# Kernel optimization log

Measured on AMD Instinct MI355X. Metric: run time of the kernel, lower is better.

## Reference

```python
import jax, jax.numpy as jnp
import numpy as np

NUM_LAYERS = 2
VOCAB = 32000
INPUT = 1024
HIDDEN = 1024
OUTPUT = 32000
BATCH = 8
SEQ = 256


def setup_inputs() -> dict:
    key = jax.random.key(0)
    ks = jax.random.split(key, 8)
    s_in = 1.0 / np.sqrt(INPUT)
    s_h = 1.0 / np.sqrt(HIDDEN)
    input_ = jax.random.randint(ks[0], (BATCH, SEQ), 0, VOCAB)
    emb = jax.random.normal(ks[1], (VOCAB, INPUT), jnp.float32)
    # Gate order along last dim: [i, f, g, o], each of width HIDDEN.
    Wx = jax.random.uniform(ks[2], (NUM_LAYERS, INPUT, 4 * HIDDEN), jnp.float32, -s_in, s_in)
    bx = jax.random.uniform(ks[3], (NUM_LAYERS, 4 * HIDDEN), jnp.float32, -s_in, s_in)
    Wh = jax.random.uniform(ks[4], (NUM_LAYERS, HIDDEN, 4 * HIDDEN), jnp.float32, -s_h, s_h)
    bh = jax.random.uniform(ks[5], (NUM_LAYERS, 4 * HIDDEN), jnp.float32, -s_h, s_h)
    Wd = jax.random.uniform(ks[6], (HIDDEN, OUTPUT), jnp.float32, -s_h, s_h)
    bd = jax.random.uniform(ks[7], (OUTPUT,), jnp.float32, -s_h, s_h)
    return {"input_": input_, "emb": emb, "Wx": Wx, "bx": bx, "Wh": Wh, "bh": bh, "Wd": Wd, "bd": bd}


def _lstm_core(input_, emb, Wx, bx, Wh, bh, Wd, bd):
    x = emb[input_]                      # [B, T, E]
    xs = jnp.swapaxes(x, 0, 1)           # [T, B, E]
    h0 = jnp.zeros((NUM_LAYERS, x.shape[0], HIDDEN), x.dtype)
    c0 = jnp.zeros_like(h0)

    def step(carry, x_t):
        h, c = carry
        layer_in = x_t
        new_h, new_c = [], []
        for l in range(NUM_LAYERS):
            gates = layer_in @ Wx[l] + bx[l] + h[l] @ Wh[l] + bh[l]  # [B, 4H]
            i_g, f_g, g_g, o_g = jnp.split(gates, 4, axis=-1)
            i_g = jax.nn.sigmoid(i_g)
            f_g = jax.nn.sigmoid(f_g)
            o_g = jax.nn.sigmoid(o_g)
            g_g = jnp.tanh(g_g)
            c_l = f_g * c[l] + i_g * g_g
            h_l = o_g * jnp.tanh(c_l)
            new_h.append(h_l)
            new_c.append(c_l)
            layer_in = h_l
        return (jnp.stack(new_h), jnp.stack(new_c)), layer_in

    (_, _), tops = jax.lax.scan(step, (h0, c0), xs)  # tops: [T, B, H]
    out = tops @ Wd + bd                              # [T, B, V]
    return jnp.swapaxes(out, 0, 1)                    # [B, T, V]


def reference(input_, emb, Wx, bx, Wh, bh, Wd, bd):
    return _lstm_core(input_, emb, Wx, bx, Wh, bh, Wd, bd)
```

## Files before the change

### kernel.cpp

```cpp
#include <hip/hip_runtime.h>
#include <cstdint>
#include <cstddef>

#define BATCH 8
#define SEQ   256
#define HID   1024
#define GATES 4096
#define VOC   32000

typedef __attribute__((ext_vector_type(8))) short bf16x8;
typedef __attribute__((ext_vector_type(4))) float f32x4;

__device__ __forceinline__ float sigf(float x){ return 1.0f/(1.0f + __expf(-x)); }
__device__ __forceinline__ float tanhf_(float x){ return 1.0f - 2.0f/(__expf(2.0f*x) + 1.0f); }

__device__ __forceinline__ unsigned short f2bf(float x){
  union { float f; unsigned u; } v; v.f = x;
  unsigned r = v.u + 0x7fffu + ((v.u >> 16) & 1u);
  return (unsigned short)(r >> 16);
}
__device__ __forceinline__ float bf2f(unsigned short h){
  union { float f; unsigned u; } v; v.u = ((unsigned)h) << 16; return v.f;
}

__global__ void k_init(unsigned* __restrict__ flags, unsigned* __restrict__ hbu){
  int tid = blockIdx.x*blockDim.x + threadIdx.x;
  int nt = gridDim.x*blockDim.x;
  for (int i = tid; i < 256*16; i += nt) flags[i] = 0u;
  for (int i = tid; i < 16384; i += nt) hbu[i] = 0u;
}

__global__ void k_wconv(const float* __restrict__ W,
                        unsigned short* __restrict__ WH){
  const int total4 = (HID*VOC) >> 2;
  int stride = gridDim.x*blockDim.x;
  for (int i = blockIdx.x*blockDim.x + threadIdx.x; i < total4; i += stride){
    float4 v = *(const float4*)(W + (size_t)i*4);
    uint2 o;
    o.x = ((unsigned)f2bf(v.x)) | (((unsigned)f2bf(v.y)) << 16);
    o.y = ((unsigned)f2bf(v.z)) | (((unsigned)f2bf(v.w)) << 16);
    *(uint2*)&WH[(size_t)i*4] = o;
  }
}

template<int AMODE, int OMODE>
__global__ __launch_bounds__(256) void k_mfma(
    const float* __restrict__ A,
    const float* __restrict__ W,
    const float* __restrict__ b1,
    const float* __restrict__ b2,
    const int*   __restrict__ tokens,
    const float* __restrict__ emb,
    float* __restrict__ C, int N)
{
  __shared__ unsigned short AsH[16*1024], AsL[16*1024];
  __shared__ unsigned short BsH[8*1024],  BsL[8*1024];
  int tid = threadIdx.x;
  int m0 = blockIdx.y*256, n0 = blockIdx.x*128;
  int w = tid >> 6, l = tid & 63;
  int lrow = l & 15, kg = l >> 4;

  f32x4 acc[4][8];
  #pragma unroll
  for (int i=0;i<4;i++){
    #pragma unroll
    for (int j=0;j<8;j++) acc[i][j] = (f32x4){0.f,0.f,0.f,0.f};
  }

  int rA  = tid >> 3, fq = tid & 7;

  const float* arow[8];
  #pragma unroll
  for (int i=0;i<8;i++){
    int gm = m0 + rA + 32*i;
    if (AMODE==1) arow[i] = emb + (size_t)tokens[(gm&7)*SEQ + (gm>>3)]*1024;
    else          arow[i] = A   + (size_t)gm*1024;
  }

  for (int kt=0; kt<32; ++kt){
    int k0 = kt*32;
    float4 av[8];
    #pragma unroll
    for (int i=0;i<8;i++)
      av[i] = *(const float4*)(arow[i] + k0 + fq*4);
    float4 wv[4];
    #pragma unroll
    for (int i=0;i<4;i++)
      wv[i] = *(const float4*)(W + (size_t)(k0 + rA)*N + n0 + fq*4 + 32*i);
    __syncthreads();
    #pragma unroll
    for (int i=0;i<8;i++){
      int r = rA + 32*i;
      int base = (r >> 4)*1024 + ((fq >> 1)*16 + (r & 15))*8 + (fq & 1)*4;
      float xs[4] = {av[i].x, av[i].y, av[i].z, av[i].w};
      unsigned long long ph = 0ull, pl = 0ull;
      #pragma unroll
      for (int c=0;c<4;c++){
        unsigned short h = f2bf(xs[c]);
        unsigned short lo = f2bf(xs[c] - bf2f(h));
        ph |= ((unsigned long long)h) << (16*c);
        pl |= ((unsigned long long)lo) << (16*c);
      }
      *(unsigned long long*)&AsH[base] = ph;
      *(unsigned long long*)&AsL[base] = pl;
    }
    #pragma unroll
    for (int i=0;i<4;i++){
      float xs[4] = {wv[i].x, wv[i].y, wv[i].z, wv[i].w};
      #pragma unroll
      for (int c=0;c<4;c++){
        int col = fq*4 + 32*i + c;
        int idx = (col >> 4)*1024 + ((rA >> 3)*16 + (col & 15))*8 + (rA & 7);
        unsigned short h = f2bf(xs[c]);
        BsH[idx] = h;
        BsL[idx] = f2bf(xs[c] - bf2f(h));
      }
    }
    __syncthreads();
    bf16x8 ah[4], al[4];
    #pragma unroll
    for (int i=0;i<4;i++){
      int fi = w*4 + i;
      ah[i] = *(const bf16x8*)&AsH[fi*1024 + l*8];
      al[i] = *(const bf16x8*)&AsL[fi*1024 + l*8];
    }
    #pragma unroll
    for (int jh=0;jh<2;jh++){
      bf16x8 bh_[4], bl_[4];
      #pragma unroll
      for (int j=0;j<4;j++){
        bh_[j] = *(const bf16x8*)&BsH[(jh*4+j)*1024 + l*8];
        bl_[j] = *(const bf16x8*)&BsL[(jh*4+j)*1024 + l*8];
      }
      #pragma unroll
      for (int i=0;i<4;i++){
        #pragma unroll
        for (int j=0;j<4;j++){
          f32x4 a = acc[i][jh*4+j];
          a = __builtin_amdgcn_mfma_f32_16x16x32_bf16(ah[i], bh_[j], a, 0,0,0);
          a = __builtin_amdgcn_mfma_f32_16x16x32_bf16(ah[i], bl_[j], a, 0,0,0);
          a = __builtin_amdgcn_mfma_f32_16x16x32_bf16(al[i], bh_[j], a, 0,0,0);
          acc[i][jh*4+j] = a;
        }
      }
    }
    __syncthreads();
  }

  int mbase = m0 + w*64 + kg*4;
  #pragma unroll
  for (int jj=0;jj<8;jj++){
    int gn = n0 + jj*16 + lrow;
    float bias = b1[gn];
    if (b2) bias += b2[gn];
    #pragma unroll
    for (int i=0;i<4;i++){
      #pragma unroll
      for (int r=0;r<4;r++){
        int m = mbase + i*16 + r;
        size_t crow = (OMODE==1) ? (size_t)((m & 7)*SEQ + (m >> 3)) : (size_t)m;
        C[crow*(size_t)N + gn] = acc[i][jj][r] + bias;
      }
    }
  }
}

__global__ __launch_bounds__(256,2) void k_proj1(
    const unsigned short* __restrict__ AH,
    const unsigned short* __restrict__ AL,
    const unsigned short* __restrict__ WH,
    const float* __restrict__ bd,
    float* __restrict__ C)
{
  __shared__ unsigned short AsH[16*1024], AsL[16*1024];
  __shared__ unsigned short BsH[8*1024];
  int tid = threadIdx.x;
  int m0 = blockIdx.y*256, n0 = blockIdx.x*128;
  int w = tid >> 6, l = tid & 63;
  int lrow = l & 15, kg = l >> 4;

  f32x4 acc[4][8];
  #pragma unroll
  for (int i=0;i<4;i++){
    #pragma unroll
    for (int j=0;j<8;j++) acc[i][j] = (f32x4){0.f,0.f,0.f,0.f};
  }

  int rA = tid >> 3, fq = tid & 7;

  uint2 avh[8], avl[8], wvh[4];
  #pragma unroll
  for (int i=0;i<8;i++){
    size_t off = (size_t)(m0 + rA + 32*i)*1024 + fq*4;
    avh[i] = *(const uint2*)&AH[off];
    avl[i] = *(const uint2*)&AL[off];
  }
  #pragma unroll
  for (int i=0;i<4;i++)
    wvh[i] = *(const uint2*)&WH[(size_t)rA*VOC + n0 + fq*4 + 32*i];

  for (int kt=0; kt<32; ++kt){
    __syncthreads();
    #pragma unroll
    for (int i=0;i<8;i++){
      int r = rA + 32*i;
      int base = (r >> 4)*1024 + ((fq >> 1)*16 + (r & 15))*8 + (fq & 1)*4;
      *(uint2*)&AsH[base] = avh[i];
      *(uint2*)&AsL[base] = avl[i];
    }
    #pragma unroll
    for (int i=0;i<4;i++){
      #pragma unroll
      for (int c=0;c<4;c++){
        int col = fq*4 + 32*i + c;
        int idx = (col >> 4)*1024 + ((rA >> 3)*16 + (col & 15))*8 + (rA & 7);
        BsH[idx] = ((const unsigned short*)&wvh[i])[c];
      }
    }
    __syncthreads();
    if (kt < 31){
      int k0 = (kt+1)*32;
      #pragma unroll
      for (int i=0;i<8;i++){
        size_t off = (size_t)(m0 + rA + 32*i)*1024 + k0 + fq*4;
        avh[i] = *(const uint2*)&AH[off];
        avl[i] = *(const uint2*)&AL[off];
      }
      #pragma unroll
      for (int i=0;i<4;i++)
        wvh[i] = *(const uint2*)&WH[(size_t)(k0 + rA)*VOC + n0 + fq*4 + 32*i];
    }
    bf16x8 ah[4], al[4];
    #pragma unroll
    for (int i=0;i<4;i++){
      int fi = w*4 + i;
      ah[i] = *(const bf16x8*)&AsH[fi*1024 + l*8];
      al[i] = *(const bf16x8*)&AsL[fi*1024 + l*8];
    }
    #pragma unroll
    for (int jh=0;jh<2;jh++){
      bf16x8 bh_[4];
      #pragma unroll
      for (int j=0;j<4;j++)
        bh_[j] = *(const bf16x8*)&BsH[(jh*4+j)*1024 + l*8];
      #pragma unroll
      for (int i=0;i<4;i++){
        #pragma unroll
        for (int j=0;j<4;j++){
          f32x4 a = acc[i][jh*4+j];
          a = __builtin_amdgcn_mfma_f32_16x16x32_bf16(ah[i], bh_[j], a, 0,0,0);
          a = __builtin_amdgcn_mfma_f32_16x16x32_bf16(al[i], bh_[j], a, 0,0,0);
          acc[i][jh*4+j] = a;
        }
      }
    }
  }
  __syncthreads();

  int mbase = m0 + w*64 + kg*4;
  #pragma unroll
  for (int jj=0;jj<8;jj++){
    int gn = n0 + jj*16 + lrow;
    float bias = bd[gn];
    #pragma unroll
    for (int i=0;i<4;i++){
      #pragma unroll
      for (int r=0;r<4;r++){
        int m = mbase + i*16 + r;
        size_t crow = (size_t)((m & 7)*SEQ + (m >> 3));
        C[crow*(size_t)VOC + gn] = acc[i][jj][r] + bias;
      }
    }
  }
}

__global__ __launch_bounds__(256) void k_proj0(
    const unsigned short* __restrict__ AH,
    const unsigned short* __restrict__ AL,
    const float* __restrict__ Wf,
    const float* __restrict__ bd,
    float* __restrict__ C)
{
  __shared__ unsigned short AsH[16*1024], AsL[16*1024];
  __shared__ unsigned short BsH[8*1024],  BsL[8*1024];
  int tid = threadIdx.x;
  int m0 = blockIdx.y*256, n0 = blockIdx.x*128;
  int w = tid >> 6, l = tid & 63;
  int lrow = l & 15, kg = l >> 4;

  f32x4 acc[4][8];
  #pragma unroll
  for (int i=0;i<4;i++){
    #pragma unroll
    for (int j=0;j<8;j++) acc[i][j] = (f32x4){0.f,0.f,0.f,0.f};
  }

  int rA = tid >> 3, fq = tid & 7;

  for (int kt=0; kt<32; ++kt){
    int k0 = kt*32;
    uint2 avh[8], avl[8];
    #pragma unroll
    for (int i=0;i<8;i++){
      size_t off = (size_t)(m0 + rA + 32*i)*1024 + k0 + fq*4;
      avh[i] = *(const uint2*)&AH[off];
      avl[i] = *(const uint2*)&AL[off];
    }
    float4 wvf[4];
    #pragma unroll
    for (int i=0;i<4;i++)
      wvf[i] = *(const float4*)(Wf + (size_t)(k0 + rA)*VOC + n0 + fq*4 + 32*i);
    __syncthreads();
    #pragma unroll
    for (int i=0;i<8;i++){
      int r = rA + 32*i;
      int base = (r >> 4)*1024 + ((fq >> 1)*16 + (r & 15))*8 + (fq & 1)*4;
      *(uint2*)&AsH[base] = avh[i];
      *(uint2*)&AsL[base] = avl[i];
    }
    #pragma unroll
    for (int i=0;i<4;i++){
      float xs[4] = {wvf[i].x, wvf[i].y, wvf[i].z, wvf[i].w};
      #pragma unroll
      for (int c=0;c<4;c++){
        int col = fq*4 + 32*i + c;
        int idx = (col >> 4)*1024 + ((rA >> 3)*16 + (col & 15))*8 + (rA & 7);
        unsigned short h = f2bf(xs[c]);
        BsH[idx] = h;
        BsL[idx] = f2bf(xs[c] - bf2f(h));
      }
    }
    __syncthreads();
    bf16x8 ah[4], al[4];
    #pragma unroll
    for (int i=0;i<4;i++){
      int fi = w*4 + i;
      ah[i] = *(const bf16x8*)&AsH[fi*1024 + l*8];
      al[i] = *(const bf16x8*)&AsL[fi*1024 + l*8];
    }
    #pragma unroll
    for (int jh=0;jh<2;jh++){
      bf16x8 bh_[4], bl_[4];
      #pragma unroll
      for (int j=0;j<4;j++){
        bh_[j] = *(const bf16x8*)&BsH[(jh*4+j)*1024 + l*8];
        bl_[j] = *(const bf16x8*)&BsL[(jh*4+j)*1024 + l*8];
      }
      #pragma unroll
      for (int i=0;i<4;i++){
        #pragma unroll
        for (int j=0;j<4;j++){
          f32x4 a = acc[i][jh*4+j];
          a = __builtin_amdgcn_mfma_f32_16x16x32_bf16(ah[i], bh_[j], a, 0,0,0);
          a = __builtin_amdgcn_mfma_f32_16x16x32_bf16(ah[i], bl_[j], a, 0,0,0);
          a = __builtin_amdgcn_mfma_f32_16x16x32_bf16(al[i], bh_[j], a, 0,0,0);
          acc[i][jh*4+j] = a;
        }
      }
    }
    __syncthreads();
  }

  int mbase = m0 + w*64 + kg*4;
  #pragma unroll
  for (int jj=0;jj<8;jj++){
    int gn = n0 + jj*16 + lrow;
    float bias = bd[gn];
    #pragma unroll
    for (int i=0;i<4;i++){
      #pragma unroll
      for (int r=0;r<4;r++){
        int m = mbase + i*16 + r;
        size_t crow = (size_t)((m & 7)*SEQ + (m >> 3));
        C[crow*(size_t)VOC + gn] = acc[i][jj][r] + bias;
      }
    }
  }
}

__global__ __launch_bounds__(256) void k_rec2(
    const float* __restrict__ G,
    const float* __restrict__ Wh,
    const float* __restrict__ Wx,
    const float* __restrict__ bx1,
    const float* __restrict__ bh1,
    unsigned short* __restrict__ TopsH,
    unsigned short* __restrict__ TopsL,
    unsigned* __restrict__ hbu,
    unsigned* __restrict__ flags)
{
  extern __shared__ char ldsb[];
  unsigned short* A0 = (unsigned short*)ldsb;
  unsigned short* A1 = A0 + 16384;
  unsigned short* A2 = A1 + 16384;
  unsigned short* hB = A2 + 16384;
  float* Cx = (float*)(ldsb + 131072);
  int tid = threadIdx.x;
  int u0 = blockIdx.x*4;
  const int wv = tid >> 6, ln = tid & 63;
  const int fs0 = tid*16, fs1 = (tid+64)*16, fs2 = (tid+128)*16, fs3 = (tid+192)*16;

  {
    int m = tid >> 4, kseg = tid & 15;
    int col = (m >> 2)*1024 + u0 + (m & 3);
    const float* wsrc[3] = { Wh, Wx + (size_t)HID*GATES, Wh + (size_t)HID*GATES };
    unsigned short* Ad[3] = { A0, A1, A2 };
    for (int tgt=0; tgt<3; ++tgt){
      const float* s = wsrc[tgt] + col;
      #pragma unroll
      for (int run=0; run<8; ++run){
        int k0 = kseg*64 + run*8;
        int kt = k0 >> 5, kg = (k0 >> 3) & 3;
        bf16x8 v;
        #pragma unroll
        for (int e=0;e<8;e++) v[e] = (short)f2bf(s[(size_t)(k0+e)*GATES]);
        *(bf16x8*)&Ad[tgt][kt*512 + ((kg<<4)|m)*8] = v;
      }
    }
  }
  float b1r[4] = {0.f,0.f,0.f,0.f};
  if (tid >= 32 && tid < 64){
    int j = tid & 3;
    #pragma unroll
    for (int g=0;g<4;g++) b1r[g] = bx1[g*1024+u0+j] + bh1[g*1024+u0+j];
  }
  float creg = 0.0f;

  for (int p=0; p<=SEQ; ++p){
    const unsigned* h0b = hbu + (size_t)(p&1)*4096;
    const unsigned* h1b = hbu + 8192 + (size_t)((p+1)&1)*4096;
    {
      int colp = tid & 15, seg0 = tid >> 4;
      #pragma unroll
      for (int i=0;i<2;i++){
        int seg = seg0 + 16*i;
        const float* src = (const float*)(((colp < 8) ? h0b : h1b)
                                          + (colp & 7)*512 + seg*16);
        float4 r0,r1,r2,r3;
        asm volatile(
          "global_load_dwordx4 %0, %4, off sc0 sc1\n\t"
          "global_load_dwordx4 %1, %4, off offset:16 sc0 sc1\n\t"
          "global_load_dwordx4 %2, %4, off offset:32 sc0 sc1\n\t"
          "global_load_dwordx4 %3, %4, off offset:48 sc0 sc1\n\t"
          "s_waitcnt vmcnt(0)"
          : "=&v"(r0),"=&v"(r1),"=&v"(r2),"=&v"(r3)
          : "v"(src)
          : "memory");
        *(float4*)&hB[seg*512 + ((0<<4)|colp)*8] = r0;
        *(float4*)&hB[seg*512 + ((1<<4)|colp)*8] = r1;
        *(float4*)&hB[seg*512 + ((2<<4)|colp)*8] = r2;
        *(float4*)&hB[seg*512 + ((3<<4)|colp)*8] = r3;
      }
    }
    float gp0=0.f,gp1=0.f,gp2=0.f,gp3=0.f;
    if (tid < 32 && p < SEQ){
      const float* gp = G + ((size_t)p*8 + (tid>>2))*GATES + u0 + (tid&3);
      gp0 = gp[0]; gp1 = gp[1024]; gp2 = gp[2048]; gp3 = gp[3072];
    }
    __syncthreads();

    f32x4 C0 = {0.f,0.f,0.f,0.f}, C1 = {0.f,0.f,0.f,0.f}, C2 = {0.f,0.f,0.f,0.f};
    #pragma unroll
    for (int kti=0; kti<8; ++kti){
      int kt = wv + kti*4;
      bf16x8 bB = *(const bf16x8*)&hB[kt*512 + ln*8];
      bf16x8 a0 = *(const bf16x8*)&A0[kt*512 + ln*8];
      bf16x8 a1 = *(const bf16x8*)&A1[kt*512 + ln*8];
      bf16x8 a2 = *(const bf16x8*)&A2[kt*512 + ln*8];
      C0 = __builtin_amdgcn_mfma_f32_16x16x32_bf16(a0, bB, C0, 0,0,0);
      C1 = __builtin_amdgcn_mfma_f32_16x16x32_bf16(a1, bB, C1, 0,0,0);
      C2 = __builtin_amdgcn_mfma_f32_16x16x32_bf16(a2, bB, C2, 0,0,0);
    }
    {
      int cn = ln & 15, mb = (ln >> 4)*4;
      #pragma unroll
      for (int r=0;r<4;r++){
        Cx[((wv*3+0)*16 + mb+r)*17 + cn] = C0[r];
        Cx[((wv*3+1)*16 + mb+r)*17 + cn] = C1[r];
        Cx[((wv*3+2)*16 + mb+r)*17 + cn] = C2[r];
      }
    }
    __syncthreads();

    float hv = 0.f; bool pub = false; unsigned dstbase = 0;
    if (tid < 32){
      if (p < SEQ){
        int b = tid >> 2, j = tid & 3;
        float gv0=gp0, gv1=gp1, gv2=gp2, gv3=gp3;
        #pragma unroll
        for (int w=0;w<4;w++){
          gv0 += Cx[((w*3+0)*16 + 0*4+j)*17 + b];
          gv1 += Cx[((w*3+0)*16 + 1*4+j)*17 + b];
          gv2 += Cx[((w*3+0)*16 + 2*4+j)*17 + b];
          gv3 += Cx[((w*3+0)*16 + 3*4+j)*17 + b];
        }
        float iv = sigf(gv0), fv = sigf(gv1), ov = sigf(gv3), gg = tanhf_(gv2);
        creg = fv*creg + iv*gg;
        hv = ov * tanhf_(creg);
        pub = true; dstbase = ((unsigned)(p+1)&1u)*4096u;
      }
    } else if (tid < 64){
      if (p > 0){
        int b = (tid-32) >> 2, j = tid & 3;
        float gv0=b1r[0], gv1=b1r[1], gv2=b1r[2], gv3=b1r[3];
        #pragma unroll
        for (int w=0;w<4;w++){
          gv0 += Cx[((w*3+1)*16 + 0*4+j)*17 + b] + Cx[((w*3+2)*16 + 0*4+j)*17 + b+8];
          gv1 += Cx[((w*3+1)*16 + 1*4+j)*17 + b] + Cx[((w*3+2)*16 + 1*4+j)*17 + b+8];
          gv2 += Cx[((w*3+1)*16 + 2*4+j)*17 + b] + Cx[((w*3+2)*16 + 2*4+j)*17 + b+8];
          gv3 += Cx[((w*3+1)*16 + 3*4+j)*17 + b] + Cx[((w*3+2)*16 + 3*4+j)*17 + b+8];
        }
        float iv = sigf(gv0), fv = sigf(gv1), ov = sigf(gv3), gg = tanhf_(gv2);
        creg = fv*creg + iv*gg;
        hv = ov * tanhf_(creg);
        pub = true; dstbase = 8192u + ((unsigned)p&1u)*4096u;
        unsigned short hi = f2bf(hv);
        unsigned short lo = f2bf(hv - bf2f(hi));
        size_t off = ((size_t)(p-1)*8 + b)*HID + u0 + (tid&3);
        TopsH[off] = hi;
        TopsL[off] = lo;
      }
    }
    if (tid < 64){
      unsigned mybits = (unsigned)f2bf(hv);
      unsigned other  = (unsigned)__shfl_xor((int)mybits, 1);
      if (pub && ((tid & 1) == 0)){
        unsigned word = (mybits & 0xffffu) | (other << 16);
        int b = (tid & 31) >> 2;
        int widx = (u0 >> 1) + ((tid >> 1) & 1);
        (void)__hip_atomic_exchange(&hbu[dstbase + b*512 + widx], word,
                                    __ATOMIC_RELAXED, __HIP_MEMORY_SCOPE_AGENT);
      }
    }

    if (p < SEQ){
      if (tid < 64){
        if (tid == 0){
          asm volatile("s_waitcnt vmcnt(0)" ::: "memory");
          (void)__hip_atomic_exchange(&flags[blockIdx.x*16], (unsigned)(p+1),
                                      __ATOMIC_RELAXED, __HIP_MEMORY_SCOPE_AGENT);
        }
        unsigned tgt = (unsigned)(p+1);
        int spins = 0;
        for (;;){
          unsigned a = __hip_atomic_load(&flags[fs0], __ATOMIC_RELAXED, __HIP_MEMORY_SCOPE_AGENT);
          unsigned b = __hip_atomic_load(&flags[fs1], __ATOMIC_RELAXED, __HIP_MEMORY_SCOPE_AGENT);
          unsigned c = __hip_atomic_load(&flags[fs2], __ATOMIC_RELAXED, __HIP_MEMORY_SCOPE_AGENT);
          unsigned d = __hip_atomic_load(&flags[fs3], __ATOMIC_RELAXED, __HIP_MEMORY_SCOPE_AGENT);
          bool ok = (a >= tgt) && (b >= tgt) && (c >= tgt) && (d >= tgt);
          if (__all(ok)) break;
          __builtin_amdgcn_s_sleep(1);
          if (++spins > 150000){
            for (;;){
              unsigned a2 = __hip_atomic_load(&flags[fs0], __ATOMIC_ACQUIRE, __HIP_MEMORY_SCOPE_AGENT);
              unsigned b2 = __hip_atomic_load(&flags[fs1], __ATOMIC_ACQUIRE, __HIP_MEMORY_SCOPE_AGENT);
              unsigned c2 = __hip_atomic_load(&flags[fs2], __ATOMIC_ACQUIRE, __HIP_MEMORY_SCOPE_AGENT);
              unsigned d2 = __hip_atomic_load(&flags[fs3], __ATOMIC_ACQUIRE, __HIP_MEMORY_SCOPE_AGENT);
              bool ok2 = (a2 >= tgt) && (b2 >= tgt) && (c2 >= tgt) && (d2 >= tgt);
              if (__all(ok2)) break;
              __builtin_amdgcn_s_sleep(8);
              if (++spins > 8000000) break;
            }
            break;
          }
        }
      }
      __syncthreads();
    }
  }
}

extern "C" void kernel_launch(void* const* d_in, const int* in_sizes, int n_in,
                              void* d_out, int out_size, void* d_ws, size_t ws_size,
                              hipStream_t stream) {
  const int*   tokens = (const int*)d_in[0];
  const float* emb = (const float*)d_in[1];
  const float* Wx  = (const float*)d_in[2];
  const float* bx  = (const float*)d_in[3];
  const float* Wh  = (const float*)d_in[4];
  const float* bh  = (const float*)d_in[5];
  const float* Wd  = (const float*)d_in[6];
  const float* bd  = (const float*)d_in[7];
  float* out = (float*)d_out;
  float* ws  = (float*)d_ws;

  float* G = ws;
  unsigned short* TopsH = (unsigned short*)(ws + (size_t)8388608);
  unsigned short* TopsL = (unsigned short*)(ws + (size_t)9437184);
  unsigned* hbu   = (unsigned*)(ws + (size_t)10485760);
  unsigned* flags = (unsigned*)(ws + (size_t)10502144);
  unsigned short* WdH = (unsigned short*)(ws + (size_t)10506240);
  const bool wpre = ws_size >= (size_t)26890240*4;

  (void)hipFuncSetAttribute((const void*)k_rec2,
        hipFuncAttributeMaxDynamicSharedMemorySize, 144128);

  k_init<<<32,256,0,stream>>>(flags, hbu);
  if (wpre)
    k_wconv<<<2048,256,0,stream>>>(Wd, WdH);

  k_mfma<1,0><<<dim3(32,8),256,0,stream>>>(nullptr, Wx, bx, bh, tokens, emb, G, GATES);

  k_rec2<<<256,256,144128,stream>>>(G, Wh, Wx, bx + GATES, bh + GATES,
                                    TopsH, TopsL, hbu, flags);

  if (wpre)
    k_proj1<<<dim3(250,8),256,0,stream>>>(TopsH, TopsL, WdH, bd, out);
  else
    k_proj0<<<dim3(250,8),256,0,stream>>>(TopsH, TopsL, Wd, bd, out);
}
```

Measured before the change: 1.738 ms.

## Fuse init and weight conversion into gate GEMM launch; batch recurrent h loads

Merges the flag/state init kernel and the Wd fp32-to-bf16 conversion into the input-gate GEMM kernel by adding 224 extra blocks that do that work alongside the GEMM blocks, removing two launches and letting the conversion run concurrently with the GEMM. In the recurrent kernel, all eight hidden-state loads are issued before a single wait, and the G gate prefetch is overlapped with them. The Tops stores are moved after the flag publish so they stay off the critical inter-block signalling path. The conversion now runs on fewer threads and shares the GPU with the GEMM, which may lengthen the pre-recurrence phase.

```diff
diff --git a/kernel.cpp b/kernel.cpp
--- a/kernel.cpp
+++ b/kernel.cpp
@@ -23,39 +23,42 @@
   union { float f; unsigned u; } v; v.u = ((unsigned)h) << 16; return v.f;
 }
 
-__global__ void k_init(unsigned* __restrict__ flags, unsigned* __restrict__ hbu){
-  int tid = blockIdx.x*blockDim.x + threadIdx.x;
-  int nt = gridDim.x*blockDim.x;
-  for (int i = tid; i < 256*16; i += nt) flags[i] = 0u;
-  for (int i = tid; i < 16384; i += nt) hbu[i] = 0u;
-}
-
-__global__ void k_wconv(const float* __restrict__ W,
-                        unsigned short* __restrict__ WH){
-  const int total4 = (HID*VOC) >> 2;
-  int stride = gridDim.x*blockDim.x;
-  for (int i = blockIdx.x*blockDim.x + threadIdx.x; i < total4; i += stride){
-    float4 v = *(const float4*)(W + (size_t)i*4);
-    uint2 o;
-    o.x = ((unsigned)f2bf(v.x)) | (((unsigned)f2bf(v.y)) << 16);
-    o.y = ((unsigned)f2bf(v.z)) | (((unsigned)f2bf(v.w)) << 16);
-    *(uint2*)&WH[(size_t)i*4] = o;
-  }
-}
-
-template<int AMODE, int OMODE>
-__global__ __launch_bounds__(256) void k_mfma(
-    const float* __restrict__ A,
+__global__ __launch_bounds__(256) void k_pre(
     const float* __restrict__ W,
     const float* __restrict__ b1,
     const float* __restrict__ b2,
     const int*   __restrict__ tokens,
     const float* __restrict__ emb,
-    float* __restrict__ C, int N)
+    float* __restrict__ C,
+    unsigned* __restrict__ flags,
+    unsigned* __restrict__ hbu,
+    const float* __restrict__ Wd,
+    unsigned short* __restrict__ WH,
+    int wpre)
 {
   __shared__ unsigned short AsH[16*1024], AsL[16*1024];
   __shared__ unsigned short BsH[8*1024],  BsL[8*1024];
   int tid = threadIdx.x;
+
+  if (blockIdx.y >= 8){
+    int sid = (blockIdx.y - 8)*32 + blockIdx.x;
+    int gtid = sid*256 + tid, nt = 224*256;
+    for (int i = gtid; i < 256*16; i += nt) flags[i] = 0u;
+    for (int i = gtid; i < 16384; i += nt) hbu[i] = 0u;
+    if (wpre){
+      const int total4 = (HID*VOC) >> 2;
+      for (int i = gtid; i < total4; i += nt){
+        float4 v = *(const float4*)(Wd + (size_t)i*4);
+        uint2 o;
+        o.x = ((unsigned)f2bf(v.x)) | (((unsigned)f2bf(v.y)) << 16);
+        o.y = ((unsigned)f2bf(v.z)) | (((unsigned)f2bf(v.w)) << 16);
+        *(uint2*)&WH[(size_t)i*4] = o;
+      }
+    }
+    return;
+  }
+
+  const int N = GATES;
   int m0 = blockIdx.y*256, n0 = blockIdx.x*128;
   int w = tid >> 6, l = tid & 63;
   int lrow = l & 15, kg = l >> 4;
@@ -73,8 +76,7 @@
   #pragma unroll
   for (int i=0;i<8;i++){
     int gm = m0 + rA + 32*i;
-    if (AMODE==1) arow[i] = emb + (size_t)tokens[(gm&7)*SEQ + (gm>>3)]*1024;
-    else          arow[i] = A   + (size_t)gm*1024;
+    arow[i] = emb + (size_t)tokens[(gm&7)*SEQ + (gm>>3)]*1024;
   }
 
   for (int kt=0; kt<32; ++kt){
@@ -151,15 +153,13 @@
   #pragma unroll
   for (int jj=0;jj<8;jj++){
     int gn = n0 + jj*16 + lrow;
-    float bias = b1[gn];
-    if (b2) bias += b2[gn];
+    float bias = b1[gn] + b2[gn];
     #pragma unroll
     for (int i=0;i<4;i++){
       #pragma unroll
       for (int r=0;r<4;r++){
         int m = mbase + i*16 + r;
-        size_t crow = (OMODE==1) ? (size_t)((m & 7)*SEQ + (m >> 3)) : (size_t)m;
-        C[crow*(size_t)N + gn] = acc[i][jj][r] + bias;
+        C[(size_t)m*N + gn] = acc[i][jj][r] + bias;
       }
     }
   }
@@ -429,33 +429,41 @@
   for (int p=0; p<=SEQ; ++p){
     const unsigned* h0b = hbu + (size_t)(p&1)*4096;
     const unsigned* h1b = hbu + 8192 + (size_t)((p+1)&1)*4096;
+    float gp0=0.f,gp1=0.f,gp2=0.f,gp3=0.f;
     {
       int colp = tid & 15, seg0 = tid >> 4;
-      #pragma unroll
-      for (int i=0;i<2;i++){
-        int seg = seg0 + 16*i;
-        const float* src = (const float*)(((colp < 8) ? h0b : h1b)
-                                          + (colp & 7)*512 + seg*16);
-        float4 r0,r1,r2,r3;
-        asm volatile(
-          "global_load_dwordx4 %0, %4, off sc0 sc1\n\t"
-          "global_load_dwordx4 %1, %4, off offset:16 sc0 sc1\n\t"
-          "global_load_dwordx4 %2, %4, off offset:32 sc0 sc1\n\t"
-          "global_load_dwordx4 %3, %4, off offset:48 sc0 sc1\n\t"
-          "s_waitcnt vmcnt(0)"
-          : "=&v"(r0),"=&v"(r1),"=&v"(r2),"=&v"(r3)
-          : "v"(src)
-          : "memory");
-        *(float4*)&hB[seg*512 + ((0<<4)|colp)*8] = r0;
-        *(float4*)&hB[seg*512 + ((1<<4)|colp)*8] = r1;
-        *(float4*)&hB[seg*512 + ((2<<4)|colp)*8] = r2;
-        *(float4*)&hB[seg*512 + ((3<<4)|colp)*8] = r3;
-      }
-    }
-    float gp0=0.f,gp1=0.f,gp2=0.f,gp3=0.f;
-    if (tid < 32 && p < SEQ){
-      const float* gp = G + ((size_t)p*8 + (tid>>2))*GATES + u0 + (tid&3);
-      gp0 = gp[0]; gp1 = gp[1024]; gp2 = gp[2048]; gp3 = gp[3072];
+      const unsigned* basep = (colp < 8) ? h0b : h1b;
+      const float* srcA = (const float*)(basep + (colp & 7)*512 + seg0*16);
+      const float* srcB = srcA + 256;
+      float4 a0,a1,a2,a3,b0,b1,b2,b3;
+      asm volatile(
+        "global_load_dwordx4 %0, %8, off sc0 sc1\n\t"
+        "global_load_dwordx4 %1, %8, off offset:16 sc0 sc1\n\t"
+        "global_load_dwordx4 %2, %8, off offset:32 sc0 sc1\n\t"
+        "global_load_dwordx4 %3, %8, off offset:48 sc0 sc1\n\t"
+        "global_load_dwordx4 %4, %9, off sc0 sc1\n\t"
+        "global_load_dwordx4 %5, %9, off offset:16 sc0 sc1\n\t"
+        "global_load_dwordx4 %6, %9, off offset:32 sc0 sc1\n\t"
+        "global_load_dwordx4 %7, %9, off offset:48 sc0 sc1"
+        : "=&v"(a0),"=&v"(a1),"=&v"(a2),"=&v"(a3),
+          "=&v"(b0),"=&v"(b1),"=&v"(b2),"=&v"(b3)
+        : "v"(srcA), "v"(srcB)
+        : "memory");
+      if (tid < 32 && p < SEQ){
+        const float* gp = G + ((size_t)p*8 + (tid>>2))*GATES + u0 + (tid&3);
+        gp0 = gp[0]; gp1 = gp[1024]; gp2 = gp[2048]; gp3 = gp[3072];
+      }
+      asm volatile("s_waitcnt vmcnt(0)" ::: "memory");
+      __builtin_amdgcn_sched_barrier(0);
+      int seg1 = seg0 + 16;
+      *(float4*)&hB[seg0*512 + ((0<<4)|colp)*8] = a0;
+      *(float4*)&hB[seg0*512 + ((1<<4)|colp)*8] = a1;
+      *(float4*)&hB[seg0*512 + ((2<<4)|colp)*8] = a2;
+      *(float4*)&hB[seg0*512 + ((3<<4)|colp)*8] = a3;
+      *(float4*)&hB[seg1*512 + ((0<<4)|colp)*8] = b0;
+      *(float4*)&hB[seg1*512 + ((1<<4)|colp)*8] = b1;
+      *(float4*)&hB[seg1*512 + ((2<<4)|colp)*8] = b2;
+      *(float4*)&hB[seg1*512 + ((3<<4)|colp)*8] = b3;
     }
     __syncthreads();
 
@@ -483,6 +491,7 @@
     __syncthreads();
 
     float hv = 0.f; bool pub = false; unsigned dstbase = 0;
+    unsigned short tH = 0, tL = 0; size_t toff = 0; bool do_tops = false;
     if (tid < 32){
       if (p < SEQ){
         int b = tid >> 2, j = tid & 3;
@@ -514,11 +523,10 @@
         creg = fv*creg + iv*gg;
         hv = ov * tanhf_(creg);
         pub = true; dstbase = 8192u + ((unsigned)p&1u)*4096u;
-        unsigned short hi = f2bf(hv);
-        unsigned short lo = f2bf(hv - bf2f(hi));
-        size_t off = ((size_t)(p-1)*8 + b)*HID + u0 + (tid&3);
-        TopsH[off] = hi;
-        TopsL[off] = lo;
+        tH = f2bf(hv);
+        tL = f2bf(hv - bf2f(tH));
+        toff = ((size_t)(p-1)*8 + b)*HID + u0 + (tid&3);
+        do_tops = true;
       }
     }
     if (tid < 64){
@@ -540,6 +548,7 @@
           (void)__hip_atomic_exchange(&flags[blockIdx.x*16], (unsigned)(p+1),
                                       __ATOMIC_RELAXED, __HIP_MEMORY_SCOPE_AGENT);
         }
+        if (do_tops){ TopsH[toff] = tH; TopsL[toff] = tL; }
         unsigned tgt = (unsigned)(p+1);
         int spins = 0;
         for (;;){
@@ -566,6 +575,8 @@
         }
       }
       __syncthreads();
+    } else {
+      if (do_tops){ TopsH[toff] = tH; TopsL[toff] = tL; }
     }
   }
 }
@@ -595,11 +606,8 @@
   (void)hipFuncSetAttribute((const void*)k_rec2,
         hipFuncAttributeMaxDynamicSharedMemorySize, 144128);
 
-  k_init<<<32,256,0,stream>>>(flags, hbu);
-  if (wpre)
-    k_wconv<<<2048,256,0,stream>>>(Wd, WdH);
-
-  k_mfma<1,0><<<dim3(32,8),256,0,stream>>>(nullptr, Wx, bx, bh, tokens, emb, G, GATES);
+  k_pre<<<dim3(32,15),256,0,stream>>>(Wx, bx, bh, tokens, emb, G,
+                                      flags, hbu, Wd, WdH, wpre ? 1 : 0);
 
   k_rec2<<<256,256,144128,stream>>>(G, Wh, Wx, bx + GATES, bh + GATES,
                                     TopsH, TopsL, hbu, flags);
```

Measured after the change: 1.811 ms. +4.2%, slower.
